# Kernel optimization log

Hardware: AMD Instinct MI355X
Metric: run time of the kernel (lower is better)

## Reference

```python
import jax, jax.numpy as jnp
import numpy as np

DIM = 768
HEADS = 12
HIDDEN = 4 * DIM
EPS = 1e-5


def _layer_norm(x, g, b):
    mu = jnp.mean(x, axis=-1, keepdims=True)
    var = jnp.mean(jnp.square(x - mu), axis=-1, keepdims=True)
    return (x - mu) * jax.lax.rsqrt(var + EPS) * g + b


def setup_inputs() -> dict:
    key = jax.random.key(0)
    ks = jax.random.split(key, 10)
    B, N, C = 16, 1024, DIM
    s = lambda fan: 1.0 / np.sqrt(fan)
    return {
        "x": jax.random.normal(ks[0], (B, N, C), dtype=jnp.float32),
        "ln1_g": jnp.ones((C,), jnp.float32),
        "ln1_b": jnp.zeros((C,), jnp.float32),
        "qkv_w": jax.random.normal(ks[1], (C, 3 * C), jnp.float32) * s(C),
        "qkv_b": jnp.zeros((3 * C,), jnp.float32),
        "proj_w": jax.random.normal(ks[2], (C, C), jnp.float32) * s(C),
        "proj_b": jnp.zeros((C,), jnp.float32),
        "ln2_g": jnp.ones((C,), jnp.float32),
        "ln2_b": jnp.zeros((C,), jnp.float32),
        "fc1_w": jax.random.normal(ks[3], (C, HIDDEN), jnp.float32) * s(C),
        "fc1_b": jnp.zeros((HIDDEN,), jnp.float32),
        "fc2_w": jax.random.normal(ks[4], (HIDDEN, C), jnp.float32) * s(HIDDEN),
        "fc2_b": jnp.zeros((C,), jnp.float32),
    }


def reference(x, ln1_g, ln1_b, qkv_w, qkv_b, proj_w, proj_b,
              ln2_g, ln2_b, fc1_w, fc1_b, fc2_w, fc2_b):
    B, N, C = x.shape
    Hd = C // HEADS
    scale = Hd ** -0.5

    # --- attention branch (pre-norm) ---
    h = _layer_norm(x, ln1_g, ln1_b)
    qkv = h @ qkv_w + qkv_b                       # [B,N,3C]
    qkv = qkv.reshape(B, N, 3, HEADS, Hd).transpose(2, 0, 3, 1, 4)
    q, k, v = qkv[0], qkv[1], qkv[2]              # [B,H,N,Hd]
    attn = jnp.einsum("bhqd,bhkd->bhqk", q, k) * scale
    attn = jax.nn.softmax(attn, axis=-1)
    o = jnp.einsum("bhqk,bhkd->bhqd", attn, v)    # [B,H,N,Hd]
    o = o.transpose(0, 2, 1, 3).reshape(B, N, C)
    x = x + (o @ proj_w + proj_b)

    # --- MLP branch (pre-norm) ---
    h = _layer_norm(x, ln2_g, ln2_b)
    h = jax.nn.gelu(h @ fc1_w + fc1_b, approximate=False)
    x = x + (h @ fc2_w + fc2_b)
    return x
```

## Files before the change

### kernel.cpp

```cpp
#include <hip/hip_runtime.h>

typedef __bf16 bf16x8 __attribute__((ext_vector_type(8)));
typedef __bf16 bf16x4 __attribute__((ext_vector_type(4)));
typedef float f32x4 __attribute__((ext_vector_type(4)));
typedef float f32x16 __attribute__((ext_vector_type(16)));

#define MFMA16(a,b,c) __builtin_amdgcn_mfma_f32_16x16x32_bf16((a),(b),(c),0,0,0)
#define MFMA32(a,b,c) __builtin_amdgcn_mfma_f32_32x32x16_bf16((a),(b),(c),0,0,0)

#define BB   16
#define SEQ  1024
#define CD   768
#define NHD  12
#define HDD  64
#define HID  3072
#define MT   (BB*SEQ)

__device__ __forceinline__ void gload16(const void* g, void* l) {
    __builtin_amdgcn_global_load_lds(
        (const __attribute__((address_space(1))) void*)g,
        (__attribute__((address_space(3))) void*)l, 16, 0, 0);
}

__device__ __forceinline__ unsigned pk2(float lo, float hi) {
    unsigned short a = __builtin_bit_cast(unsigned short, (__bf16)lo);
    unsigned short b = __builtin_bit_cast(unsigned short, (__bf16)hi);
    return (unsigned)a | ((unsigned)b << 16);
}

__device__ __forceinline__ float fast_gelu(float x) {
    float u = x * x * x;
    float y = fmaf(0.044715f, u, x);
    float e = __builtin_amdgcn_exp2f(-2.3022083f * y);
    return x * __builtin_amdgcn_rcpf(1.0f + e);
}

__global__ __launch_bounds__(256)
void transpose_w(const float* __restrict__ W, __bf16* __restrict__ WT, int R, int C)
{
    __shared__ float t[32][33];
    int tc = C >> 5;
    int bid = blockIdx.x;
    int br = bid / tc, bc = bid % tc;
    int x = threadIdx.x & 31, y = threadIdx.x >> 5;
#pragma unroll
    for (int i = 0; i < 4; ++i)
        t[y + 8*i][x] = W[(size_t)(br*32 + y + 8*i)*C + bc*32 + x];
    __syncthreads();
#pragma unroll
    for (int i = 0; i < 4; ++i)
        WT[(size_t)(bc*32 + y + 8*i)*R + br*32 + x] = (__bf16)t[x][y + 8*i];
}

__global__ __launch_bounds__(256)
void ln_kernel(const float* __restrict__ xin, const float* __restrict__ g,
               const float* __restrict__ bb, __bf16* out)
{
    int row = blockIdx.x * 4 + (threadIdx.x >> 6);
    int lane = threadIdx.x & 63;
    const float* xr = xin + (size_t)row * CD + lane * 4;
    float4 v0 = *(const float4*)(xr);
    float4 v1 = *(const float4*)(xr + 256);
    float4 v2 = *(const float4*)(xr + 512);
    float s = v0.x+v0.y+v0.z+v0.w + v1.x+v1.y+v1.z+v1.w + v2.x+v2.y+v2.z+v2.w;
#pragma unroll
    for (int off = 1; off < 64; off <<= 1) s += __shfl_xor(s, off);
    float mu = s * (1.0f/768.0f);
    float q =
        (v0.x-mu)*(v0.x-mu)+(v0.y-mu)*(v0.y-mu)+(v0.z-mu)*(v0.z-mu)+(v0.w-mu)*(v0.w-mu)+
        (v1.x-mu)*(v1.x-mu)+(v1.y-mu)*(v1.y-mu)+(v1.z-mu)*(v1.z-mu)+(v1.w-mu)*(v1.w-mu)+
        (v2.x-mu)*(v2.x-mu)+(v2.y-mu)*(v2.y-mu)+(v2.z-mu)*(v2.z-mu)+(v2.w-mu)*(v2.w-mu);
#pragma unroll
    for (int off = 1; off < 64; off <<= 1) q += __shfl_xor(q, off);
    float rstd = rsqrtf(q * (1.0f/768.0f) + 1e-5f);

    __bf16* orow = out + (size_t)row * CD + lane * 4;
#pragma unroll
    for (int p = 0; p < 3; ++p) {
        float4 xv = (p == 0) ? v0 : (p == 1) ? v1 : v2;
        float4 gv = *(const float4*)(g  + p*256 + lane*4);
        float4 bv = *(const float4*)(bb + p*256 + lane*4);
        bf16x4 ov;
        ov[0] = (__bf16)((xv.x-mu)*rstd*gv.x + bv.x);
        ov[1] = (__bf16)((xv.y-mu)*rstd*gv.y + bv.y);
        ov[2] = (__bf16)((xv.z-mu)*rstd*gv.z + bv.z);
        ov[3] = (__bf16)((xv.w-mu)*rstd*gv.w + bv.w);
        *(bf16x4*)(orow + p*256) = ov;
    }
}

template<int EPI>
__global__ __launch_bounds__(256)
void gemm_bt(const __bf16* __restrict__ A, const __bf16* __restrict__ BT,
             const float* __restrict__ bias,
             const float* res, float* outf,
             __bf16* __restrict__ outb,
             __bf16* __restrict__ qb, __bf16* __restrict__ kb, __bf16* __restrict__ vb,
             int M, int N, int K)
{
    __shared__ alignas(16) __bf16 lsA[2][128*64];
    __shared__ alignas(16) __bf16 lsB[2][128*64];

    int nbn = N >> 7;
    int nwg = (M >> 7) * nbn;
    int bid = (int)blockIdx.x;
    int cpx = nwg >> 3;
    int sw = (bid & 7) * cpx + (bid >> 3);
    int bm = sw / nbn, bn = sw % nbn;
    int row0 = bm << 7, col0 = bn << 7;

    int tid = threadIdx.x;
    int lane = tid & 63, w = tid >> 6;
    int wr = w >> 1, wc = w & 1;
    int lr = lane & 15, lg = lane >> 4;

    f32x4 acc[4][4] = {};
    int sbase = w * 4096 + lane * 16;
    int swz = (lr & 7) << 4;

    auto stage = [&](int buf, int ktE) {
#pragma unroll
        for (int i = 0; i < 4; ++i) {
            int s = sbase + (i << 10);
            int r = s >> 7;
            int ch = ((s >> 4) & 7) ^ (r & 7);
            gload16(A  + (size_t)(row0 + r)*K + (ktE + ch*8),
                    (char*)lsA + buf*16384 + (w*4 + i)*1024);
            gload16(BT + (size_t)(col0 + r)*K + (ktE + ch*8),
                    (char*)lsB + buf*16384 + (w*4 + i)*1024);
        }
    };

    int nkt = K >> 6;
    stage(0, 0);
    __syncthreads();
    int cur = 0;

    for (int kt = 0; kt < nkt; ++kt) {
        if (kt + 1 < nkt) stage(cur ^ 1, (kt + 1) << 6);

        const char* lA = (const char*)lsA + cur*16384;
        const char* lB = (const char*)lsB + cur*16384;
#pragma unroll
        for (int ks = 0; ks < 2; ++ks) {
            int cb = (ks*64 + lg*16) ^ swz;
            bf16x8 af[4], bfv[4];
#pragma unroll
            for (int m = 0; m < 4; ++m) {
                af[m]  = *(const bf16x8*)(lA + (wr*64 + m*16 + lr)*128 + cb);
                bfv[m] = *(const bf16x8*)(lB + (wc*64 + m*16 + lr)*128 + cb);
            }
#pragma unroll
            for (int m = 0; m < 4; ++m)
#pragma unroll
                for (int n = 0; n < 4; ++n)
                    acc[m][n] = MFMA16(af[m], bfv[n], acc[m][n]);
        }
        __syncthreads();
        cur ^= 1;
    }

    int rbase = row0 + wr*64 + lg*4;
    int cbase = col0 + wc*64 + lr;
#pragma unroll
    for (int n = 0; n < 4; ++n) {
        int col = cbase + n*16;
        float bv = bias[col];
        if constexpr (EPI == 0) {
            int which = col / CD;
            int c2 = col - which * CD;
            int head = c2 >> 6, d = c2 & 63;
#pragma unroll
            for (int m = 0; m < 4; ++m) {
                int r0 = rbase + m*16;
                int b = r0 >> 10, nn = r0 & 1023;
                if (which == 2) {
                    bf16x4 pv;
#pragma unroll
                    for (int j = 0; j < 4; ++j) pv[j] = (__bf16)(acc[m][n][j] + bv);
                    *(bf16x4*)&vb[(((size_t)b*NHD + head)*HDD + d)*SEQ + nn] = pv;
                } else {
                    __bf16* dst = (which == 0) ? qb : kb;
#pragma unroll
                    for (int j = 0; j < 4; ++j)
                        dst[(((size_t)b*NHD + head)*SEQ + nn + j)*HDD + d] =
                            (__bf16)(acc[m][n][j] + bv);
                }
            }
        } else {
#pragma unroll
            for (int m = 0; m < 4; ++m) {
                int rr = rbase + m*16;
#pragma unroll
                for (int j = 0; j < 4; ++j) {
                    float val = acc[m][n][j] + bv;
                    int r = rr + j;
                    if constexpr (EPI == 1) {
                        outf[(size_t)r*N + col] = res[(size_t)r*N + col] + val;
                    } else {
                        outb[(size_t)r*N + col] = (__bf16)fast_gelu(val);
                    }
                }
            }
        }
    }
}

__global__ __launch_bounds__(256)
void attn_kernel(const __bf16* __restrict__ q, const __bf16* __restrict__ k,
                 const __bf16* __restrict__ vT, __bf16* __restrict__ o)
{
    __shared__ alignas(16) __bf16 kls[2][64*64];
    __shared__ alignas(16) __bf16 vls[2][64*64];

    int bid = blockIdx.x;
    int bh = bid % (BB*NHD);
    int qt = bid / (BB*NHD);
    int b = bh / NHD, hh = bh % NHD;
    int tid = threadIdx.x, lane = tid & 63, w = tid >> 6;
    int lq = lane & 31, h = lane >> 5;

    int qg = qt*128 + w*32 + lq;
    const __bf16* qp = q + ((size_t)bh*SEQ + qg)*HDD + h*8;
    bf16x8 qf[4];
#pragma unroll
    for (int s = 0; s < 4; ++s) qf[s] = *(const bf16x8*)(qp + s*16);

    const __bf16* kbase = k  + (size_t)bh*SEQ*HDD;
    const __bf16* vbase = vT + (size_t)bh*HDD*SEQ;

    int srow0 = tid >> 3;
    int scol0 = ((tid & 7) ^ (srow0 & 7)) * 8;
    int srow1 = srow0 + 32;

    auto stage = [&](int buf, int kv) {
        char* kl = (char*)kls + buf*8192 + w*1024;
        char* vl = (char*)vls + buf*8192 + w*1024;
        gload16(kbase + (size_t)(kv + srow0)*HDD + scol0, kl);
        gload16(kbase + (size_t)(kv + srow1)*HDD + scol0, kl + 4096);
        gload16(vbase + (size_t)srow0*SEQ + kv + scol0, vl);
        gload16(vbase + (size_t)srow1*SEQ + kv + scol0, vl + 4096);
    };

    const float SCL2 = 0.125f * 1.44269504f;
    float mrun = -1e30f, lrun = 0.f;
    f32x16 oa0 = {}, oa1 = {};

    stage(0, 0);
    __syncthreads();
    int cur = 0;
    int rswz = (lq & 7) << 4;

    for (int kt = 0; kt < SEQ/64; ++kt) {
        if (kt + 1 < SEQ/64) stage(cur ^ 1, (kt + 1)*64);

        const char* kc = (const char*)kls + cur*8192;
        const char* vc = (const char*)vls + cur*8192;

        bf16x8 ka0[4], ka1[4];
#pragma unroll
        for (int s = 0; s < 4; ++s) {
            int bc = (h*16 + s*32) ^ rswz;
            ka0[s] = *(const bf16x8*)(kc + lq*128 + bc);
            ka1[s] = *(const bf16x8*)(kc + (lq + 32)*128 + bc);
        }
        bf16x8 vf0[4], vf1[4];
#pragma unroll
        for (int g = 0; g < 4; ++g) {
            int bc = (h*16 + g*32) ^ rswz;
            vf0[g] = *(const bf16x8*)(vc + lq*128 + bc);
            vf1[g] = *(const bf16x8*)(vc + (lq + 32)*128 + bc);
        }

        f32x16 s0 = {}, s1 = {};
        __builtin_amdgcn_s_setprio(1);
#pragma unroll
        for (int s = 0; s < 4; ++s) {
            s0 = MFMA32(ka0[s], qf[s], s0);
            s1 = MFMA32(ka1[s], qf[s], s1);
        }
        __builtin_amdgcn_s_setprio(0);

        float tm = s0[0];
#pragma unroll
        for (int i = 1; i < 16; ++i) tm = fmaxf(tm, s0[i]);
#pragma unroll
        for (int i = 0; i < 16; ++i) tm = fmaxf(tm, s1[i]);
        tm = fmaxf(tm, __shfl_xor(tm, 32));
        if (!__all(tm <= mrun)) {
            float mnew = fmaxf(mrun, tm);
            float alpha = exp2f((mrun - mnew) * SCL2);
            mrun = mnew;
            lrun *= alpha;
            oa0 = oa0 * alpha;
            oa1 = oa1 * alpha;
        }
        float nb = -mrun * SCL2;
        float ts = 0.f;
#pragma unroll
        for (int i = 0; i < 16; ++i) { s0[i] = exp2f(fmaf(s0[i], SCL2, nb)); ts += s0[i]; }
#pragma unroll
        for (int i = 0; i < 16; ++i) { s1[i] = exp2f(fmaf(s1[i], SCL2, nb)); ts += s1[i]; }
        ts += __shfl_xor(ts, 32);
        lrun += ts;

#pragma unroll
        for (int t = 0; t < 2; ++t) {
            const f32x16& sp = t ? s1 : s0;
            unsigned d0 = pk2(sp[ 0], sp[ 1]);
            unsigned d1 = pk2(sp[ 2], sp[ 3]);
            unsigned d2 = pk2(sp[ 4], sp[ 5]);
            unsigned d3 = pk2(sp[ 6], sp[ 7]);
            unsigned d4 = pk2(sp[ 8], sp[ 9]);
            unsigned d5 = pk2(sp[10], sp[11]);
            unsigned d6 = pk2(sp[12], sp[13]);
            unsigned d7 = pk2(sp[14], sp[15]);
            unsigned pd0 = __shfl_xor(d0, 32), pd1 = __shfl_xor(d1, 32);
            unsigned pd2 = __shfl_xor(d2, 32), pd3 = __shfl_xor(d3, 32);
            unsigned pd4 = __shfl_xor(d4, 32), pd5 = __shfl_xor(d5, 32);
            unsigned pd6 = __shfl_xor(d6, 32), pd7 = __shfl_xor(d7, 32);
            union { unsigned u[4]; bf16x8 v; } f0, f1;
            f0.u[0] = h ? pd2 : d0;
            f0.u[1] = h ? pd3 : d1;
            f0.u[2] = h ? d2 : pd0;
            f0.u[3] = h ? d3 : pd1;
            f1.u[0] = h ? pd6 : d4;
            f1.u[1] = h ? pd7 : d5;
            f1.u[2] = h ? d6 : pd4;
            f1.u[3] = h ? d7 : pd5;
            __builtin_amdgcn_s_setprio(1);
            oa0 = MFMA32(vf0[t*2 + 0], f0.v, oa0);
            oa1 = MFMA32(vf1[t*2 + 0], f0.v, oa1);
            oa0 = MFMA32(vf0[t*2 + 1], f1.v, oa0);
            oa1 = MFMA32(vf1[t*2 + 1], f1.v, oa1);
            __builtin_amdgcn_s_setprio(0);
        }

        __syncthreads();
        cur ^= 1;
    }

    float inv = 1.0f / lrun;
    oa0 = oa0 * inv;
    oa1 = oa1 * inv;
    __bf16* orow = o + ((size_t)b*SEQ + qg)*CD + hh*HDD;
#pragma unroll
    for (int dt = 0; dt < 2; ++dt) {
        f32x16 oa = dt ? oa1 : oa0;
        unsigned d0 = pk2(oa[ 0], oa[ 1]);
        unsigned d1 = pk2(oa[ 2], oa[ 3]);
        unsigned d2 = pk2(oa[ 4], oa[ 5]);
        unsigned d3 = pk2(oa[ 6], oa[ 7]);
        unsigned d4 = pk2(oa[ 8], oa[ 9]);
        unsigned d5 = pk2(oa[10], oa[11]);
        unsigned d6 = pk2(oa[12], oa[13]);
        unsigned d7 = pk2(oa[14], oa[15]);
        unsigned pd0 = __shfl_xor(d0, 32), pd1 = __shfl_xor(d1, 32);
        unsigned pd2 = __shfl_xor(d2, 32), pd3 = __shfl_xor(d3, 32);
        unsigned pd4 = __shfl_xor(d4, 32), pd5 = __shfl_xor(d5, 32);
        unsigned pd6 = __shfl_xor(d6, 32), pd7 = __shfl_xor(d7, 32);
        union { unsigned u[4]; bf16x8 v; } g0, g1;
        g0.u[0] = h ? pd2 : d0;
        g0.u[1] = h ? pd3 : d1;
        g0.u[2] = h ? d2 : pd0;
        g0.u[3] = h ? d3 : pd1;
        g1.u[0] = h ? pd6 : d4;
        g1.u[1] = h ? pd7 : d5;
        g1.u[2] = h ? d6 : pd4;
        g1.u[3] = h ? d7 : pd5;
        *(bf16x8*)(orow + dt*32 +  0 + h*8) = g0.v;
        *(bf16x8*)(orow + dt*32 + 16 + h*8) = g1.v;
    }
}

extern "C" void kernel_launch(void* const* d_in, const int* in_sizes, int n_in,
                              void* d_out, int out_size, void* d_ws, size_t ws_size,
                              hipStream_t stream)
{
    const float* x     = (const float*)d_in[0];
    const float* ln1g  = (const float*)d_in[1];
    const float* ln1b  = (const float*)d_in[2];
    const float* qkvw  = (const float*)d_in[3];
    const float* qkvb  = (const float*)d_in[4];
    const float* projw = (const float*)d_in[5];
    const float* projb = (const float*)d_in[6];
    const float* ln2g  = (const float*)d_in[7];
    const float* ln2b  = (const float*)d_in[8];
    const float* fc1w  = (const float*)d_in[9];
    const float* fc1b  = (const float*)d_in[10];
    const float* fc2w  = (const float*)d_in[11];
    const float* fc2b  = (const float*)d_in[12];
    float* out = (float*)d_out;

    char* p = (char*)d_ws;
    auto alloc = [&](size_t bytes) { char* r = p; p += (bytes + 255) & ~(size_t)255; return r; };
    __bf16* wqkvT  = (__bf16*)alloc((size_t)3*CD*CD*2);
    __bf16* wprojT = (__bf16*)alloc((size_t)CD*CD*2);
    __bf16* wfc1T  = (__bf16*)alloc((size_t)HID*CD*2);
    __bf16* wfc2T  = (__bf16*)alloc((size_t)CD*HID*2);
    __bf16* hbuf   = (__bf16*)alloc((size_t)MT*CD*2);
    __bf16* qbuf   = (__bf16*)alloc((size_t)BB*NHD*SEQ*HDD*2);
    __bf16* kbuf   = (__bf16*)alloc((size_t)BB*NHD*SEQ*HDD*2);
    __bf16* vtbuf  = (__bf16*)alloc((size_t)BB*NHD*SEQ*HDD*2);
    (void)alloc((size_t)BB*NHD*SEQ*HDD*2);
    __bf16* hhbuf  = qbuf;

    transpose_w<<<(CD/32)*(3*CD/32), 256, 0, stream>>>(qkvw,  wqkvT, CD, 3*CD);
    transpose_w<<<(CD/32)*(CD/32),   256, 0, stream>>>(projw, wprojT, CD, CD);
    transpose_w<<<(CD/32)*(HID/32),  256, 0, stream>>>(fc1w,  wfc1T, CD, HID);
    transpose_w<<<(HID/32)*(CD/32),  256, 0, stream>>>(fc2w,  wfc2T, HID, CD);

    ln_kernel<<<MT/4, 256, 0, stream>>>(x, ln1g, ln1b, hbuf);

    gemm_bt<0><<<(MT/128)*(3*CD/128), 256, 0, stream>>>(
        hbuf, wqkvT, qkvb, nullptr, nullptr, nullptr, qbuf, kbuf, vtbuf, MT, 3*CD, CD);

    attn_kernel<<<BB*NHD*8, 256, 0, stream>>>(qbuf, kbuf, vtbuf, hbuf);

    gemm_bt<1><<<(MT/128)*(CD/128), 256, 0, stream>>>(
        hbuf, wprojT, projb, x, out, nullptr, nullptr, nullptr, nullptr, MT, CD, CD);

    ln_kernel<<<MT/4, 256, 0, stream>>>(out, ln2g, ln2b, hbuf);

    gemm_bt<2><<<(MT/128)*(HID/128), 256, 0, stream>>>(
        hbuf, wfc1T, fc1b, nullptr, nullptr, hhbuf, nullptr, nullptr, nullptr, MT, HID, CD);

    gemm_bt<1><<<(MT/128)*(CD/128), 256, 0, stream>>>(
        hhbuf, wfc2T, fc2b, out, out, nullptr, nullptr, nullptr, nullptr, MT, CD, HID);
}
```

Measured before the change: 485.5 us.

## Use partial vmcnt waits with raw barriers and tree reductions in GEMM and attention

Replaces the full __syncthreads in the GEMM and flash-attention main loops with an explicit s_waitcnt vmcnt(N) plus a raw s_barrier. Each iteration then waits only for the current tile's global-to-LDS loads while the next tile's prefetch stays in flight. The softmax max and sum reductions become tree reductions to shorten dependency chains, and exp2f and the final division are swapped for the raw hardware exp2 and rcp intrinsics. The hand-written waitcnt counts depend on how many loads each stage issues, and the raw intrinsics drop the denormal and range handling of exp2f and the exact division.

```diff
diff --git a/kernel.cpp b/kernel.cpp
--- a/kernel.cpp
+++ b/kernel.cpp
@@ -7,6 +7,7 @@
 
 #define MFMA16(a,b,c) __builtin_amdgcn_mfma_f32_16x16x32_bf16((a),(b),(c),0,0,0)
 #define MFMA32(a,b,c) __builtin_amdgcn_mfma_f32_32x32x16_bf16((a),(b),(c),0,0,0)
+#define EXP2R(x) __builtin_amdgcn_exp2f(x)
 
 #define BB   16
 #define SEQ  1024
@@ -31,7 +32,7 @@
 __device__ __forceinline__ float fast_gelu(float x) {
     float u = x * x * x;
     float y = fmaf(0.044715f, u, x);
-    float e = __builtin_amdgcn_exp2f(-2.3022083f * y);
+    float e = EXP2R(-2.3022083f * y);
     return x * __builtin_amdgcn_rcpf(1.0f + e);
 }
 
@@ -133,11 +134,16 @@
 
     int nkt = K >> 6;
     stage(0, 0);
-    __syncthreads();
-    int cur = 0;
 
     for (int kt = 0; kt < nkt; ++kt) {
-        if (kt + 1 < nkt) stage(cur ^ 1, (kt + 1) << 6);
+        int cur = kt & 1;
+        if (kt + 1 < nkt) {
+            stage(cur ^ 1, (kt + 1) << 6);
+            asm volatile("s_waitcnt vmcnt(8)" ::: "memory");
+        } else {
+            asm volatile("s_waitcnt vmcnt(0)" ::: "memory");
+        }
+        __builtin_amdgcn_s_barrier();
 
         const char* lA = (const char*)lsA + cur*16384;
         const char* lB = (const char*)lsB + cur*16384;
@@ -156,8 +162,9 @@
                 for (int n = 0; n < 4; ++n)
                     acc[m][n] = MFMA16(af[m], bfv[n], acc[m][n]);
         }
-        __syncthreads();
-        cur ^= 1;
+        asm volatile("s_waitcnt lgkmcnt(0)" ::: "memory");
+        __builtin_amdgcn_sched_barrier(0);
+        __builtin_amdgcn_s_barrier();
     }
 
     int rbase = row0 + wr*64 + lg*4;
@@ -247,12 +254,17 @@
     f32x16 oa0 = {}, oa1 = {};
 
     stage(0, 0);
-    __syncthreads();
-    int cur = 0;
     int rswz = (lq & 7) << 4;
 
     for (int kt = 0; kt < SEQ/64; ++kt) {
-        if (kt + 1 < SEQ/64) stage(cur ^ 1, (kt + 1)*64);
+        int cur = kt & 1;
+        if (kt + 1 < SEQ/64) {
+            stage(cur ^ 1, (kt + 1)*64);
+            asm volatile("s_waitcnt vmcnt(4)" ::: "memory");
+        } else {
+            asm volatile("s_waitcnt vmcnt(0)" ::: "memory");
+        }
+        __builtin_amdgcn_s_barrier();
 
         const char* kc = (const char*)kls + cur*8192;
         const char* vc = (const char*)vls + cur*8192;
@@ -281,26 +293,34 @@
         }
         __builtin_amdgcn_s_setprio(0);
 
-        float tm = s0[0];
-#pragma unroll
-        for (int i = 1; i < 16; ++i) tm = fmaxf(tm, s0[i]);
-#pragma unroll
-        for (int i = 0; i < 16; ++i) tm = fmaxf(tm, s1[i]);
+        float t8[8];
+#pragma unroll
+        for (int i = 0; i < 8; ++i)
+            t8[i] = fmaxf(fmaxf(s0[i], s0[i + 8]), fmaxf(s1[i], s1[i + 8]));
+        float t4a = fmaxf(fmaxf(t8[0], t8[1]), fmaxf(t8[2], t8[3]));
+        float t4b = fmaxf(fmaxf(t8[4], t8[5]), fmaxf(t8[6], t8[7]));
+        float tm = fmaxf(t4a, t4b);
         tm = fmaxf(tm, __shfl_xor(tm, 32));
         if (!__all(tm <= mrun)) {
             float mnew = fmaxf(mrun, tm);
-            float alpha = exp2f((mrun - mnew) * SCL2);
+            float alpha = EXP2R((mrun - mnew) * SCL2);
             mrun = mnew;
             lrun *= alpha;
             oa0 = oa0 * alpha;
             oa1 = oa1 * alpha;
         }
         float nb = -mrun * SCL2;
-        float ts = 0.f;
-#pragma unroll
-        for (int i = 0; i < 16; ++i) { s0[i] = exp2f(fmaf(s0[i], SCL2, nb)); ts += s0[i]; }
-#pragma unroll
-        for (int i = 0; i < 16; ++i) { s1[i] = exp2f(fmaf(s1[i], SCL2, nb)); ts += s1[i]; }
+#pragma unroll
+        for (int i = 0; i < 16; ++i) s0[i] = EXP2R(fmaf(s0[i], SCL2, nb));
+#pragma unroll
+        for (int i = 0; i < 16; ++i) s1[i] = EXP2R(fmaf(s1[i], SCL2, nb));
+        float a8[8];
+#pragma unroll
+        for (int i = 0; i < 8; ++i)
+            a8[i] = (s0[i] + s0[i + 8]) + (s1[i] + s1[i + 8]);
+        float s4a = (a8[0] + a8[1]) + (a8[2] + a8[3]);
+        float s4b = (a8[4] + a8[5]) + (a8[6] + a8[7]);
+        float ts = s4a + s4b;
         ts += __shfl_xor(ts, 32);
         lrun += ts;
 
@@ -336,11 +356,12 @@
             __builtin_amdgcn_s_setprio(0);
         }
 
-        __syncthreads();
-        cur ^= 1;
+        asm volatile("s_waitcnt lgkmcnt(0)" ::: "memory");
+        __builtin_amdgcn_sched_barrier(0);
+        __builtin_amdgcn_s_barrier();
     }
 
-    float inv = 1.0f / lrun;
+    float inv = __builtin_amdgcn_rcpf(lrun);
     oa0 = oa0 * inv;
     oa1 = oa1 * inv;
     __bf16* orow = o + ((size_t)b*SEQ + qg)*CD + hh*HDD;
```

Result: slower. 519.6 us (+7.0%).
